# Kernel optimization log

Measured on AMD Instinct MI355X. Metric: run time of the kernel, lower is better.

The kernel has to match this reference:

```python
import jax, jax.numpy as jnp
import numpy as np
import math

B = 32768
AMP = 1.0 / math.sqrt(2.0 * math.pi)
PRETRAIN_EPOCH = 2
BETA_W, THETA_W, TWIST_W, UVD24_W, XYZ24_W = 1.0, 0.01, 0.01, 1.0, 1.0


def setup_inputs() -> dict:
    key = jax.random.key(0)
    ks = jax.random.split(key, 24)
    rn = lambda k, s: jax.random.normal(k, s, dtype=jnp.float32)
    ru = lambda k, s: jax.random.uniform(k, s, dtype=jnp.float32)
    return {
        "pred_shape": rn(ks[0], (B, 10)),
        "pred_theta_mats": rn(ks[1], (B, 216)),
        "pred_phi": rn(ks[2], (B, 23, 2)),
        "pred_xyz_jts_29": rn(ks[3], (B, 87)),
        # shifted so per-sample loss_uvd sums straddle 0 (keeps masking loop nontrivial)
        "nf_loss": rn(ks[4], (B, 96, 3)) - 1.8,
        # sigma in (0.5, 1.5): positive, well-conditioned log
        "sigma": ru(ks[5], (B, 96, 3)) + 0.5,
        "pred_uvd_jts": rn(ks[6], (B, 29, 3)),
        "pred_uvd_mks": rn(ks[7], (B, 67, 3)),
        "cam_trans": rn(ks[8], (B, 2)),
        "cam_scale": rn(ks[9], (B, 1)),
        "target_smpl_weight": ru(ks[10], (B, 1)),
        "target_beta": rn(ks[11], (B, 10)),
        "target_theta": rn(ks[12], (B, 216)),
        "target_theta_weight": ru(ks[13], (B, 216)),
        "target_twist": rn(ks[14], (B, 23, 2)),
        "target_twist_weight": ru(ks[15], (B, 23, 2)),
        "target_xyz_24": rn(ks[16], (B, 72)),
        "target_xyz_weight_24": ru(ks[17], (B, 72)),
        "target_uvd_29": rn(ks[18], (B, 87)),
        "target_uvd_67": rn(ks[19], (B, 201)),
        "target_weight_29": ru(ks[20], (B, 87)),
        "target_weight_67": ru(ks[21], (B, 201)),
        "camera_trans": rn(ks[22], (B, 2)),
        "camera_scale": rn(ks[23], (B, 1)),
        "epoch_num": 5,
    }


def _mse(a, b):
    return jnp.mean(jnp.square(a - b))


def _weighted_l1(inp, tgt, w):
    out = jnp.abs(inp * 64.0 - tgt * 64.0) * w
    s, ws = out.sum(), w.sum()
    return jnp.where(ws > 0, s / ws, s)


def reference(pred_shape, pred_theta_mats, pred_phi, pred_xyz_jts_29, nf_loss, sigma,
              pred_uvd_jts, pred_uvd_mks, cam_trans, cam_scale,
              target_smpl_weight, target_beta, target_theta, target_theta_weight,
              target_twist, target_twist_weight, target_xyz_24, target_xyz_weight_24,
              target_uvd_29, target_uvd_67, target_weight_29, target_weight_67,
              camera_trans, camera_scale, epoch_num):
    sw = target_smpl_weight  # [B,1]
    loss_beta = _mse(pred_shape * sw, target_beta * sw)
    loss_theta = _mse(pred_theta_mats * sw * target_theta_weight,
                      target_theta * sw * target_theta_weight)
    loss_twist = _mse(pred_phi * target_twist_weight, target_twist * target_twist_weight)

    pred_xyz = pred_xyz_jts_29[:, :72]
    txw = target_xyz_weight_24[:, :72]
    loss_xyz = _weighted_l1(pred_xyz, target_xyz_24[:, :72], txw)

    # concat 29 joints + 67 markers -> [B, 96, 3]
    pred_uvd = jnp.concatenate([pred_uvd_jts, pred_uvd_mks], axis=1)
    tgt_uvd = jnp.concatenate([target_uvd_29.reshape(pred_uvd_jts.shape),
                               target_uvd_67.reshape(pred_uvd_mks.shape)], axis=1)
    w_uvd = jnp.concatenate([target_weight_29.reshape(pred_uvd_jts.shape),
                             target_weight_67.reshape(pred_uvd_mks.shape)], axis=1)

    q_logprob = (jnp.log(sigma / AMP)
                 + jnp.abs(tgt_uvd - pred_uvd) / (math.sqrt(2.0) * sigma + 1e-9)) * w_uvd
    loss_uvd = nf_loss * w_uvd + q_logprob  # [B,96,3]

    # size_average path (vectorized form of the per-sample masking loop)
    if epoch_num > 0:
        per_sample = loss_uvd.sum(axis=(1, 2))          # [B]
        keep = (per_sample <= 0).astype(loss_uvd.dtype)  # loop zeroes samples with sum > 0
        used = keep.sum()
        masked_sum = (loss_uvd * keep[:, None, None]).sum()
    else:
        used = jnp.asarray(float(loss_uvd.shape[0]), loss_uvd.dtype)
        masked_sum = loss_uvd.sum()
    loss_uvd_scalar = jnp.where(w_uvd.sum() > 0, masked_sum / used, loss_uvd.sum())

    loss = loss_beta * BETA_W + loss_theta * THETA_W + loss_twist * TWIST_W
    if epoch_num > PRETRAIN_EPOCH:
        loss = loss + loss_xyz * XYZ24_W
    loss = loss + loss_uvd_scalar * UVD24_W

    sw2 = (txw.sum(axis=1) > 3).astype(jnp.float32)[:, None]  # [B,1]
    trans_loss = _mse(cam_trans * sw2, camera_trans * sw2)
    scale_loss = _mse(cam_scale * sw2, camera_scale * sw2)
    cam_coef = 0.1 if epoch_num > PRETRAIN_EPOCH else 1.0
    loss = loss + cam_coef * (trans_loss + scale_loss)

    return (loss, loss_uvd_scalar, loss_beta, loss_theta, loss_twist, trans_loss, scale_loss)
```

## Files before the change

kernel.cpp:

```cpp
#include <hip/hip_runtime.h>
#include <math.h>

#define NB 32768
#define NACC 11
#define MAXBLOCKS 2048
#define NTHREADS 256
#define WAVES_PER_BLOCK (NTHREADS / 64)


__device__ __forceinline__ float wave_sum(float v) {
#pragma unroll
    for (int off = 1; off < 64; off <<= 1)
        v += __shfl_xor(v, off, 64);
    return v;
}

__device__ __forceinline__ float4 ld4(const float* p) {
    return *reinterpret_cast<const float4*>(p);
}

__global__ __launch_bounds__(NTHREADS) void fused_loss_kernel(
    const float* __restrict__ pred_shape,
    const float* __restrict__ pred_theta_mats,
    const float* __restrict__ pred_phi,
    const float* __restrict__ pred_xyz_jts_29,
    const float* __restrict__ nf_loss,
    const float* __restrict__ sigma,
    const float* __restrict__ pred_uvd_jts,
    const float* __restrict__ pred_uvd_mks,
    const float* __restrict__ cam_trans,
    const float* __restrict__ cam_scale,
    const float* __restrict__ target_smpl_weight,
    const float* __restrict__ target_beta,
    const float* __restrict__ target_theta,
    const float* __restrict__ target_theta_weight,
    const float* __restrict__ target_twist,
    const float* __restrict__ target_twist_weight,
    const float* __restrict__ target_xyz_24,
    const float* __restrict__ target_xyz_weight_24,
    const float* __restrict__ target_uvd_29,
    const float* __restrict__ target_uvd_67,
    const float* __restrict__ target_weight_29,
    const float* __restrict__ target_weight_67,
    const float* __restrict__ camera_trans,
    const float* __restrict__ camera_scale,
    float* __restrict__ partials)
{
    const int lane = threadIdx.x & 63;
    const int widx = threadIdx.x >> 6;
    const int wave_id = blockIdx.x * WAVES_PER_BLOCK + widx;
    const int nwaves = gridDim.x * WAVES_PER_BLOCK;

    const float INV_AMP = 2.5066282746310002f;
    const float SQRT2   = 1.4142135623730951f;

    float acc[NACC];
#pragma unroll
    for (int i = 0; i < NACC; ++i) acc[i] = 0.f;

    for (int b = wave_id; b < NB; b += nwaves) {
        const float sw = target_smpl_weight[b];

        if (lane < 10) {
            float p = pred_shape[b * 10 + lane];
            float t = target_beta[b * 10 + lane];
            float d = p * sw - t * sw;
            acc[0] += d * d;
        }

        if (lane < 54) {
            int off = b * 216 + lane * 4;
            float4 p = ld4(pred_theta_mats + off);
            float4 t = ld4(target_theta + off);
            float4 w = ld4(target_theta_weight + off);
            float d;
            d = p.x * sw * w.x - t.x * sw * w.x; acc[1] += d * d;
            d = p.y * sw * w.y - t.y * sw * w.y; acc[1] += d * d;
            d = p.z * sw * w.z - t.z * sw * w.z; acc[1] += d * d;
            d = p.w * sw * w.w - t.w * sw * w.w; acc[1] += d * d;
        }

        if (lane < 46) {
            int off = b * 46 + lane;
            float p = pred_phi[off];
            float t = target_twist[off];
            float w = target_twist_weight[off];
            float d = p * w - t * w;
            acc[2] += d * d;
        }

        float rw = 0.f;
        if (lane < 18) {
            int off = b * 72 + lane * 4;
            float4 t = ld4(target_xyz_24 + off);
            float4 w = ld4(target_xyz_weight_24 + off);
            const float* pp = pred_xyz_jts_29 + b * 87 + lane * 4;
            float ta[4] = {t.x, t.y, t.z, t.w};
            float wa[4] = {w.x, w.y, w.z, w.w};
#pragma unroll
            for (int k = 0; k < 4; ++k) {
                float p = pp[k];
                float d = fabsf(p * 64.f - ta[k] * 64.f) * wa[k];
                acc[3] += d;
                rw += wa[k];
            }
        }
        acc[4] += rw;
        float row_w = wave_sum(rw);
        float sw2 = (row_w > 3.f) ? 1.f : 0.f;

        if (lane < 2) {
            float p = cam_trans[b * 2 + lane];
            float t = camera_trans[b * 2 + lane];
            float d = p * sw2 - t * sw2;
            acc[9] += d * d;
        }
        if (lane == 0) {
            float p = cam_scale[b];
            float t = camera_scale[b];
            float d = p * sw2 - t * sw2;
            acc[10] += d * d;
        }

        const float* nf_row = nf_loss + (size_t)b * 288;
        const float* sg_row = sigma   + (size_t)b * 288;
        float samp = 0.f;
#pragma unroll
        for (int it = 0; it < 2; ++it) {
            int j = it * 256 + lane * 4;
            if (j < 288) {
                float4 nf = ld4(nf_row + j);
                float4 sg = ld4(sg_row + j);
                float nfa[4] = {nf.x, nf.y, nf.z, nf.w};
                float sga[4] = {sg.x, sg.y, sg.z, sg.w};
#pragma unroll
                for (int k = 0; k < 4; ++k) {
                    int jj = j + k;
                    float p, t, w;
                    if (jj < 87) {
                        int o = b * 87 + jj;
                        p = pred_uvd_jts[o];
                        t = target_uvd_29[o];
                        w = target_weight_29[o];
                    } else {
                        int o = b * 201 + (jj - 87);
                        p = pred_uvd_mks[o];
                        t = target_uvd_67[o];
                        w = target_weight_67[o];
                    }
                    float s = sga[k];
                    float q = (logf(s * INV_AMP) +
                               fabsf(t - p) / (SQRT2 * s + 1e-9f)) * w;
                    float e = nfa[k] * w + q;
                    samp += e;
                    acc[7] += w;
                }
            }
        }
        acc[8] += samp;
        float s_uvd = wave_sum(samp);
        if (lane == 0 && s_uvd <= 0.f) {
            acc[5] += s_uvd;
            acc[6] += 1.f;
        }
    }

    __shared__ float sacc[WAVES_PER_BLOCK][NACC];
#pragma unroll
    for (int i = 0; i < NACC; ++i) {
        float v = wave_sum(acc[i]);
        if (lane == 0) sacc[widx][i] = v;
    }
    __syncthreads();
    if (threadIdx.x < NACC) {
        float v = 0.f;
#pragma unroll
        for (int w = 0; w < WAVES_PER_BLOCK; ++w) v += sacc[w][threadIdx.x];
        partials[blockIdx.x * NACC + threadIdx.x] = v;
    }
}

__global__ __launch_bounds__(256) void finalize_kernel(
    const float* __restrict__ partials, int nblocks,
    const int* __restrict__ epoch_num_p, float* __restrict__ out)
{
    const int lane = threadIdx.x & 63;
    const int widx = threadIdx.x >> 6;
    __shared__ float sums[NACC];

    for (int i = widx; i < NACC; i += 4) {
        float v = 0.f;
        for (int p = lane; p < nblocks; p += 64)
            v += partials[p * NACC + i];
        v = wave_sum(v);
        if (lane == 0) sums[i] = v;
    }
    __syncthreads();

    if (threadIdx.x == 0) {
        const int epoch = epoch_num_p[0];
        const float Bf = (float)NB;

        float loss_beta  = sums[0] / (Bf * 10.f);
        float loss_theta = sums[1] / (Bf * 216.f);
        float loss_twist = sums[2] / (Bf * 46.f);
        float loss_xyz   = (sums[4] > 0.f) ? (sums[3] / sums[4]) : sums[3];

        float ms = (epoch > 0) ? sums[5] : sums[8];
        float us = (epoch > 0) ? sums[6] : Bf;
        float loss_uvd = (sums[7] > 0.f) ? (ms / us) : sums[8];

        float trans_loss = sums[9] / (Bf * 2.f);
        float scale_loss = sums[10] / Bf;

        float loss = loss_beta * 1.0f + loss_theta * 0.01f + loss_twist * 0.01f;
        if (epoch > 2) loss += loss_xyz * 1.0f;
        loss += loss_uvd * 1.0f;
        float cam_coef = (epoch > 2) ? 0.1f : 1.0f;
        loss = loss + cam_coef * (trans_loss + scale_loss);

        out[0] = loss;
        out[1] = loss_uvd;
        out[2] = loss_beta;
        out[3] = loss_theta;
        out[4] = loss_twist;
        out[5] = trans_loss;
        out[6] = scale_loss;
    }
}

extern "C" void kernel_launch(void* const* d_in, const int* in_sizes, int n_in,
                              void* d_out, int out_size, void* d_ws, size_t ws_size,
                              hipStream_t stream) {
    (void)in_sizes; (void)n_in; (void)out_size;

    int nblocks = MAXBLOCKS;
    size_t need = (size_t)nblocks * NACC * sizeof(float);
    if (ws_size < need) nblocks = (int)(ws_size / (NACC * sizeof(float)));
    if (nblocks < 1) nblocks = 1;

    float* partials = (float*)d_ws;

    fused_loss_kernel<<<nblocks, NTHREADS, 0, stream>>>(
        (const float*)d_in[0],  (const float*)d_in[1],  (const float*)d_in[2],
        (const float*)d_in[3],  (const float*)d_in[4],  (const float*)d_in[5],
        (const float*)d_in[6],  (const float*)d_in[7],  (const float*)d_in[8],
        (const float*)d_in[9],  (const float*)d_in[10], (const float*)d_in[11],
        (const float*)d_in[12], (const float*)d_in[13], (const float*)d_in[14],
        (const float*)d_in[15], (const float*)d_in[16], (const float*)d_in[17],
        (const float*)d_in[18], (const float*)d_in[19], (const float*)d_in[20],
        (const float*)d_in[21], (const float*)d_in[22], (const float*)d_in[23],
        partials);

    finalize_kernel<<<1, 256, 0, stream>>>(
        partials, nblocks, (const int*)d_in[24], (float*)d_out);
}
```

Measured before the change: 362.0 us.

## Use lane-contiguous scalar loads for xyz/uvd rows and transpose partials layout

Replaces the per-lane float4 plus strided scalar access in the xyz and uvd sections with lane-contiguous scalar loads, so each wave instruction touches consecutive addresses. This is meant to improve coalescing of the pred/target/weight gathers, which were previously strided by four per lane. The partials buffer becomes accumulator-major, and the finalize kernel now reads each accumulator with all 256 threads instead of one wave per accumulator. Splitting the uvd work into five iterations gives more loop trips and more select logic per element.

```diff
diff --git a/kernel.cpp b/kernel.cpp
--- a/kernel.cpp
+++ b/kernel.cpp
@@ -89,79 +89,70 @@
             acc[2] += d * d;
         }
 
-        float rw = 0.f;
-        if (lane < 18) {
-            int off = b * 72 + lane * 4;
-            float4 t = ld4(target_xyz_24 + off);
-            float4 w = ld4(target_xyz_weight_24 + off);
-            const float* pp = pred_xyz_jts_29 + b * 87 + lane * 4;
-            float ta[4] = {t.x, t.y, t.z, t.w};
-            float wa[4] = {w.x, w.y, w.z, w.w};
-#pragma unroll
-            for (int k = 0; k < 4; ++k) {
-                float p = pp[k];
-                float d = fabsf(p * 64.f - ta[k] * 64.f) * wa[k];
-                acc[3] += d;
-                rw += wa[k];
-            }
-        }
-        acc[4] += rw;
-        float row_w = wave_sum(rw);
-        float sw2 = (row_w > 3.f) ? 1.f : 0.f;
-
-        if (lane < 2) {
-            float p = cam_trans[b * 2 + lane];
-            float t = camera_trans[b * 2 + lane];
-            float d = p * sw2 - t * sw2;
-            acc[9] += d * d;
-        }
-        if (lane == 0) {
-            float p = cam_scale[b];
-            float t = camera_scale[b];
-            float d = p * sw2 - t * sw2;
-            acc[10] += d * d;
-        }
-
-        const float* nf_row = nf_loss + (size_t)b * 288;
-        const float* sg_row = sigma   + (size_t)b * 288;
-        float samp = 0.f;
-#pragma unroll
-        for (int it = 0; it < 2; ++it) {
-            int j = it * 256 + lane * 4;
-            if (j < 288) {
-                float4 nf = ld4(nf_row + j);
-                float4 sg = ld4(sg_row + j);
-                float nfa[4] = {nf.x, nf.y, nf.z, nf.w};
-                float sga[4] = {sg.x, sg.y, sg.z, sg.w};
-#pragma unroll
-                for (int k = 0; k < 4; ++k) {
-                    int jj = j + k;
-                    float p, t, w;
-                    if (jj < 87) {
-                        int o = b * 87 + jj;
-                        p = pred_uvd_jts[o];
-                        t = target_uvd_29[o];
-                        w = target_weight_29[o];
-                    } else {
-                        int o = b * 201 + (jj - 87);
-                        p = pred_uvd_mks[o];
-                        t = target_uvd_67[o];
-                        w = target_weight_67[o];
-                    }
-                    float s = sga[k];
-                    float q = (logf(s * INV_AMP) +
-                               fabsf(t - p) / (SQRT2 * s + 1e-9f)) * w;
-                    float e = nfa[k] * w + q;
-                    samp += e;
+        {
+            const int oxyz = b * 72;
+            const int opx  = b * 87;
+            float rw = 0.f;
+#pragma unroll
+            for (int it = 0; it < 2; ++it) {
+                int j = it * 64 + lane;
+                if (j < 72) {
+                    float t = target_xyz_24[oxyz + j];
+                    float w = target_xyz_weight_24[oxyz + j];
+                    float p = pred_xyz_jts_29[opx + j];
+                    acc[3] += fabsf(p * 64.f - t * 64.f) * w;
+                    rw += w;
+                }
+            }
+            acc[4] += rw;
+            float row_w = wave_sum(rw);
+            float sw2 = (row_w > 3.f) ? 1.f : 0.f;
+
+            if (lane < 2) {
+                float p = cam_trans[b * 2 + lane];
+                float t = camera_trans[b * 2 + lane];
+                float d = p * sw2 - t * sw2;
+                acc[9] += d * d;
+            }
+            if (lane == 0) {
+                float p = cam_scale[b];
+                float t = camera_scale[b];
+                float d = p * sw2 - t * sw2;
+                acc[10] += d * d;
+            }
+        }
+
+        {
+            const float* nf_row = nf_loss + (size_t)b * 288;
+            const float* sg_row = sigma   + (size_t)b * 288;
+            const int oj = b * 87;
+            const int om = b * 201 - 87;
+            float samp = 0.f;
+#pragma unroll
+            for (int it = 0; it < 5; ++it) {
+                int j = it * 64 + lane;
+                if (j < 288) {
+                    float nf = nf_row[j];
+                    float sg = sg_row[j];
+                    bool isj = (j < 87);
+                    const float* P = isj ? (pred_uvd_jts    + oj) : (pred_uvd_mks    + om);
+                    const float* T = isj ? (target_uvd_29   + oj) : (target_uvd_67   + om);
+                    const float* W = isj ? (target_weight_29 + oj) : (target_weight_67 + om);
+                    float p = P[j];
+                    float t = T[j];
+                    float w = W[j];
+                    float q = (logf(sg * INV_AMP) +
+                               fabsf(t - p) / (SQRT2 * sg + 1e-9f)) * w;
+                    samp += nf * w + q;
                     acc[7] += w;
                 }
             }
-        }
-        acc[8] += samp;
-        float s_uvd = wave_sum(samp);
-        if (lane == 0 && s_uvd <= 0.f) {
-            acc[5] += s_uvd;
-            acc[6] += 1.f;
+            acc[8] += samp;
+            float s_uvd = wave_sum(samp);
+            if (lane == 0 && s_uvd <= 0.f) {
+                acc[5] += s_uvd;
+                acc[6] += 1.f;
+            }
         }
     }
 
@@ -176,28 +167,42 @@
         float v = 0.f;
 #pragma unroll
         for (int w = 0; w < WAVES_PER_BLOCK; ++w) v += sacc[w][threadIdx.x];
-        partials[blockIdx.x * NACC + threadIdx.x] = v;
-    }
-}
-
-__global__ __launch_bounds__(256) void finalize_kernel(
+        partials[threadIdx.x * gridDim.x + blockIdx.x] = v;
+    }
+}
+
+__global__ __launch_bounds__(NTHREADS) void finalize_kernel(
     const float* __restrict__ partials, int nblocks,
     const int* __restrict__ epoch_num_p, float* __restrict__ out)
 {
-    const int lane = threadIdx.x & 63;
-    const int widx = threadIdx.x >> 6;
-    __shared__ float sums[NACC];
-
-    for (int i = widx; i < NACC; i += 4) {
-        float v = 0.f;
-        for (int p = lane; p < nblocks; p += 64)
-            v += partials[p * NACC + i];
-        v = wave_sum(v);
-        if (lane == 0) sums[i] = v;
+    const int tid  = threadIdx.x;
+    const int lane = tid & 63;
+    const int widx = tid >> 6;
+
+    float a[NACC];
+#pragma unroll
+    for (int i = 0; i < NACC; ++i) a[i] = 0.f;
+
+    for (int p = tid; p < nblocks; p += NTHREADS) {
+#pragma unroll
+        for (int i = 0; i < NACC; ++i)
+            a[i] += partials[i * nblocks + p];
+    }
+
+    __shared__ float red[NACC][WAVES_PER_BLOCK];
+#pragma unroll
+    for (int i = 0; i < NACC; ++i) {
+        float v = wave_sum(a[i]);
+        if (lane == 0) red[i][widx] = v;
     }
     __syncthreads();
 
-    if (threadIdx.x == 0) {
+    if (tid == 0) {
+        float sums[NACC];
+#pragma unroll
+        for (int i = 0; i < NACC; ++i)
+            sums[i] = red[i][0] + red[i][1] + red[i][2] + red[i][3];
+
         const int epoch = epoch_num_p[0];
         const float Bf = (float)NB;
 
@@ -252,6 +257,6 @@
         (const float*)d_in[21], (const float*)d_in[22], (const float*)d_in[23],
         partials);
 
-    finalize_kernel<<<1, 256, 0, stream>>>(
+    finalize_kernel<<<1, NTHREADS, 0, stream>>>(
         partials, nblocks, (const int*)d_in[24], (float*)d_out);
 }
```

Measured after the change: 344.3 us. 1.05x faster.
